# Kernel tuning notes

Measured on AMD Instinct MI355X. Metric: run time of the kernel, lower is better.

Reference implementation:

```python
import jax, jax.numpy as jnp
import numpy as np

L, B, IN, H, OUT = 4, 4096, 1024, 1024, 1024


def setup_inputs() -> dict:
    key = jax.random.key(0)
    ks = jax.random.split(key, 9)
    std = 1.0 / (H + IN) ** 0.5
    return {
        "x": jax.random.normal(ks[0], (B, IN), jnp.float32),
        "h_prev": jax.random.normal(ks[1], (L, B, H), jnp.float32),
        "c_prev": jax.random.normal(ks[2], (L, B, H), jnp.float32),
        "Wi": jax.random.uniform(ks[3], (L, IN, 4 * H), jnp.float32, -std, std),
        "Wh": jax.random.uniform(ks[4], (L, H, 4 * H), jnp.float32, -std, std),
        "bi": jax.random.uniform(ks[5], (L, 4 * H), jnp.float32, -std, std),
        "bh": jax.random.uniform(ks[6], (L, 4 * H), jnp.float32, -std, std),
        "fc_W": jax.random.uniform(ks[7], (H, OUT), jnp.float32, -std, std),
        "fc_b": jax.random.uniform(ks[8], (OUT,), jnp.float32, -std, std),
    }


def _lstm_cell(x, h, c, Wi, Wh, bi, bh):
    # gates: [B, 4H], split into (input, forget, cell, output)
    gates = x @ Wi + bi + h @ Wh + bh
    i, f, g, o = jnp.split(gates, 4, axis=1)
    i, f, o = jax.nn.sigmoid(i), jax.nn.sigmoid(f), jax.nn.sigmoid(o)
    g = jnp.tanh(g)
    c_cur = f * c + i * g
    h_cur = o * jnp.tanh(c_cur)
    return h_cur, c_cur


def reference(x, h_prev, c_prev, Wi, Wh, bi, bh, fc_W, fc_b):
    h_out, c_out = [], []
    x_in = x
    for l in range(L):  # fixed small layer loop
        h_cur, c_cur = _lstm_cell(x_in, h_prev[l], c_prev[l], Wi[l], Wh[l], bi[l], bh[l])
        h_out.append(h_cur)
        c_out.append(c_cur)
        x_in = h_cur
    h_out = jnp.stack(h_out, axis=0)
    c_out = jnp.stack(c_out, axis=0)
    y = h_out[-1] @ fc_W + fc_b
    return y, h_out, c_out
```

## Files before the change

### kernel.cpp

```cpp
#include <hip/hip_runtime.h>

#define B_    4096
#define H_    1024
#define NLAY  4

typedef __attribute__((ext_vector_type(8))) short bf16x8;
typedef __attribute__((ext_vector_type(4))) short s16x4;
typedef __attribute__((ext_vector_type(4))) float f32x4;
typedef unsigned short ushort_t;

__device__ __forceinline__ ushort_t f2bf(float f) {
  unsigned u = __builtin_bit_cast(unsigned, f);
  u += 0x7FFFu + ((u >> 16) & 1u);
  return (ushort_t)(u >> 16);
}

__device__ __forceinline__ float fast_sigmoid(float x) {
  float e = __expf(-fabsf(x));
  float s = 1.0f / (1.0f + e);
  return x >= 0.0f ? s : 1.0f - s;
}
__device__ __forceinline__ float fast_tanh(float x) {
  float e = __expf(-2.0f * fabsf(x));
  float t = (1.0f - e) / (1.0f + e);
  return x >= 0.0f ? t : -t;
}

#define GLDS16(gsrc, ldst)                                                  \
  __builtin_amdgcn_global_load_lds(                                         \
      (__attribute__((address_space(1))) void*)(gsrc),                      \
      (__attribute__((address_space(3))) void*)(ldst), 16, 0, 0)

#define BAR()                                                               \
  { asm volatile("" ::: "memory");                                          \
    __builtin_amdgcn_s_barrier();                                           \
    asm volatile("" ::: "memory"); }

#define WAITV(N)                                                            \
  { asm volatile("s_waitcnt vmcnt(" #N ")" ::: "memory");                   \
    __builtin_amdgcn_sched_barrier(0); }

#define LGKM0()                                                             \
  { asm volatile("s_waitcnt lgkmcnt(0)" ::: "memory");                      \
    __builtin_amdgcn_sched_barrier(0); }

__device__ __forceinline__ bf16x8 dsr128(unsigned addr, int imm) {
  bf16x8 r;
  asm volatile("ds_read_b128 %0, %1 offset:%c2"
               : "=v"(r)
               : "v"(addr), "i"(imm));
  return r;
}

__global__ __launch_bounds__(256, 1) void lstm8(
    const ushort_t* __restrict__ aX, const ushort_t* __restrict__ aH,
    const float* __restrict__ cprev, const float* __restrict__ bi,
    const float* __restrict__ bh, const ushort_t* __restrict__ wtl,
    float* __restrict__ hout, float* __restrict__ cout,
    ushort_t* __restrict__ hbfout) {
  __shared__ __align__(16) char sL[131072];

  const int tid  = threadIdx.x;
  const int lane = tid & 63;
  const int wid  = tid >> 6;
  const int wm   = wid >> 1;
  const int wn   = wid & 1;
  const int xcd = blockIdx.x & 7, bj = blockIdx.x >> 3;
  const int bm  = (xcd >> 2) * 8 + (bj >> 2);
  const int bn  = (xcd & 3) * 4 + (bj & 3);

  const int fr = lane & 15;
  const int oF = lane >> 4;
  const int sw = (oF ^ ((fr >> 1) & 3)) * 16;

  const unsigned sBase = (unsigned)(size_t)&sL[0];
  const unsigned aAddr = sBase + (unsigned)(wm * 16384 + fr * 64 + sw);
  const unsigned bAddr = sBase + (unsigned)(65536 + wn * 16384 + fr * 64 + sw);

  int aof[4];
#pragma unroll
  for (int c = 0; c < 4; ++c) {
    const int q = tid + c * 256;
    const int kh = q >> 9, r = (q >> 2) & 127, s = q & 3;
    const int o = s ^ ((r >> 1) & 3);
    aof[c] = r * 1024 + kh * 32 + o * 8;
  }
  const int aof0 = aof[0], aof1 = aof[1], aof2 = aof[2], aof3 = aof[3];
  const size_t aRowBase = (size_t)(bm * 256) * 1024;
  const ushort_t* wtBn = wtl + (size_t)bn * 524288;

  f32x4 acc[8][8];
#pragma unroll
  for (int m = 0; m < 8; ++m)
#pragma unroll
    for (int n = 0; n < 8; ++n) acc[m][n] = (f32x4){0.f, 0.f, 0.f, 0.f};

  bf16x8 ar[4][2], br0[4][2], br1[4][2];

#define STAGE_A(PAR, HALF, TT)                                               \
  {                                                                          \
    const ushort_t* bp = (((TT) < 16) ? aX : aH) + aRowBase +                \
                         (HALF) * 131072 + ((TT) & 15) * 64;                 \
    char* d = sL + (PAR) * 32768 + (HALF) * 16384 + wid * 1024;              \
    GLDS16(bp + aof0, d);                                                    \
    GLDS16(bp + aof1, d + 4096);                                             \
    GLDS16(bp + aof2, d + 8192);                                             \
    GLDS16(bp + aof3, d + 12288);                                            \
  }
#define STAGE_B(PAR, HALF, TT)                                               \
  {                                                                          \
    const ushort_t* bp =                                                     \
        wtBn + (size_t)(TT) * 16384 + (HALF) * 8192 + tid * 8;               \
    char* d = sL + 65536 + (PAR) * 32768 + (HALF) * 16384 + wid * 1024;      \
    GLDS16(bp, d);                                                           \
    GLDS16(bp + 2048, d + 4096);                                             \
    GLDS16(bp + 4096, d + 8192);                                             \
    GLDS16(bp + 6144, d + 12288);                                            \
  }
#define RD_A(PAR, MH)                                                        \
  _Pragma("unroll") for (int mp = 0; mp < 4; ++mp)                           \
      _Pragma("unroll") for (int kh = 0; kh < 2; ++kh)                       \
      ar[mp][kh] = dsr128(aAddr, (PAR) * 32768 + kh * 8192 +                 \
                                     ((MH) * 4 + mp) * 1024);
#define RD_B(PAR, NH, BR)                                                    \
  _Pragma("unroll") for (int gg = 0; gg < 4; ++gg)                           \
      _Pragma("unroll") for (int kh = 0; kh < 2; ++kh)                       \
      BR[gg][kh] = dsr128(bAddr, (PAR) * 32768 + kh * 8192 +                 \
                                     ((NH) * 4 + gg) * 1024);
#define MM(MH, NH, BR)                                                       \
  _Pragma("unroll") for (int gg = 0; gg < 4; ++gg)                           \
      _Pragma("unroll") for (int mp = 0; mp < 4; ++mp)                       \
      _Pragma("unroll") for (int kh = 0; kh < 2; ++kh)                       \
      acc[(MH) * 4 + mp][(NH) * 4 + gg] =                                    \
          __builtin_amdgcn_mfma_f32_16x16x32_bf16(                           \
              ar[mp][kh], BR[gg][kh], acc[(MH) * 4 + mp][(NH) * 4 + gg],     \
              0, 0, 0);

  STAGE_A(0, 0, 0)
  STAGE_A(0, 1, 0)
  STAGE_B(0, 0, 0)
  STAGE_B(0, 1, 0)
  STAGE_B(1, 0, 1)
  STAGE_B(1, 1, 1)
  WAITV(8)
  BAR()

#pragma unroll 1
  for (int t2 = 0; t2 < 32; t2 += 2) {
    RD_A(0, 0) RD_B(0, 0, br0)
    STAGE_A(1, 0, t2 + 1)
    BAR()
    LGKM0()
    MM(0, 0, br0)
    BAR()

    RD_B(0, 1, br1)
    STAGE_A(1, 1, t2 + 1)
    BAR()
    LGKM0()
    MM(0, 1, br1)
    BAR()

    RD_A(0, 1)
    STAGE_B(0, 0, t2 + 2)
    BAR()
    LGKM0()
    MM(1, 0, br0)
    BAR()

    STAGE_B(0, 1, t2 + 2)
    BAR()
    MM(1, 1, br1)
    WAITV(8)
    BAR()

    RD_A(1, 0) RD_B(1, 0, br0)
    STAGE_A(0, 0, t2 + 2)
    BAR()
    LGKM0()
    MM(0, 0, br0)
    BAR()

    RD_B(1, 1, br1)
    STAGE_A(0, 1, t2 + 2)
    BAR()
    LGKM0()
    MM(0, 1, br1)
    BAR()

    RD_A(1, 1)
    STAGE_B(1, 0, t2 + 3)
    BAR()
    LGKM0()
    MM(1, 0, br0)
    BAR()

    STAGE_B(1, 1, t2 + 3)
    BAR()
    MM(1, 1, br1)
    WAITV(8)
    BAR()
  }
#undef STAGE_A
#undef STAGE_B
#undef RD_A
#undef RD_B
#undef MM

  WAITV(0)
  __syncthreads();

  float bsum[2][4];
#pragma unroll
  for (int hg = 0; hg < 2; ++hg)
#pragma unroll
    for (int g = 0; g < 4; ++g) {
      const int col = g * 1024 + bn * 64 + wn * 32 + hg * 16 + fr;
      bsum[hg][g] = bi[col] + bh[col];
    }

#define LSTRIDE 68
  float* LF = (float*)sL;
  const int crow = tid >> 4;
  const int cc4  = (tid & 15) * 4;
  {
    const float* cp0 = cprev + (size_t)(bm * 256) * 1024 + bn * 64;
#pragma unroll
    for (int i = 0; i < 16; ++i) {
      const int row = i * 16 + crow;
      f32x4 v = *(const f32x4*)(cp0 + (size_t)row * 1024 + cc4);
      *(f32x4*)(LF + row * LSTRIDE + cc4) = v;
    }
  }
  __syncthreads();
  float hv[8][2][4];
#pragma unroll
  for (int m = 0; m < 8; ++m) {
    const int rowb = wm * 128 + m * 16 + oF * 4;
#pragma unroll
    for (int hg = 0; hg < 2; ++hg) {
      const int hc = wn * 32 + hg * 16 + fr;
#pragma unroll
      for (int r = 0; r < 4; ++r) {
        const float cp = LF[(rowb + r) * LSTRIDE + hc];
        const float gi = fast_sigmoid(acc[m][0 + hg][r] + bsum[hg][0]);
        const float gf = fast_sigmoid(acc[m][2 + hg][r] + bsum[hg][1]);
        const float gg = fast_tanh(acc[m][4 + hg][r] + bsum[hg][2]);
        const float go = fast_sigmoid(acc[m][6 + hg][r] + bsum[hg][3]);
        const float c  = gf * cp + gi * gg;
        LF[(rowb + r) * LSTRIDE + hc] = c;
        hv[m][hg][r] = go * fast_tanh(c);
      }
    }
  }
  __syncthreads();
  {
    float* co0 = cout + (size_t)(bm * 256) * 1024 + bn * 64;
#pragma unroll
    for (int i = 0; i < 16; ++i) {
      const int row = i * 16 + crow;
      f32x4 v = *(const f32x4*)(LF + row * LSTRIDE + cc4);
      *(f32x4*)(co0 + (size_t)row * 1024 + cc4) = v;
    }
  }
  __syncthreads();
#pragma unroll
  for (int m = 0; m < 8; ++m) {
    const int rowb = wm * 128 + m * 16 + oF * 4;
#pragma unroll
    for (int hg = 0; hg < 2; ++hg) {
      const int hc = wn * 32 + hg * 16 + fr;
#pragma unroll
      for (int r = 0; r < 4; ++r) LF[(rowb + r) * LSTRIDE + hc] = hv[m][hg][r];
    }
  }
  __syncthreads();
  {
    float* ho0 = hout + (size_t)(bm * 256) * 1024 + bn * 64;
    ushort_t* hb0 = hbfout + (size_t)(bm * 256) * 1024 + bn * 64;
#pragma unroll
    for (int i = 0; i < 16; ++i) {
      const int row = i * 16 + crow;
      f32x4 v = *(const f32x4*)(LF + row * LSTRIDE + cc4);
      *(f32x4*)(ho0 + (size_t)row * 1024 + cc4) = v;
      s16x4 hb;
#pragma unroll
      for (int j = 0; j < 4; ++j) hb[j] = (short)f2bf(v[j]);
      *(s16x4*)(hb0 + (size_t)row * 1024 + cc4) = hb;
    }
  }
#undef LSTRIDE
}

__global__ __launch_bounds__(512) void packW(const float* __restrict__ Wi,
                                             const float* __restrict__ Wh,
                                             ushort_t* __restrict__ wt) {
  __shared__ ushort_t t16[64 * 256];
  const int bn = blockIdx.x;
  const int T  = blockIdx.y;
  const int l  = blockIdx.z;
  const int tid = threadIdx.x;
  const int kq = tid >> 6, cc = tid & 63;
  const int k0 = T * 64;
  const float* W = (k0 < 1024)
                       ? (Wi + (size_t)l * 1024 * 4096 + (size_t)k0 * 4096)
                       : (Wh + (size_t)l * 1024 * 4096 + (size_t)(k0 - 1024) * 4096);
#pragma unroll
  for (int kk = 0; kk < 8; ++kk) {
    const int kl = kq * 8 + kk;
#pragma unroll
    for (int g = 0; g < 4; ++g) {
      const float v = W[(size_t)kl * 4096 + g * 1024 + bn * 64 + cc];
      const int p = (cc >> 5) * 128 + g * 32 + ((cc >> 4) & 1) * 16 + (cc & 15);
      t16[kl * 256 + p] = f2bf(v);
    }
  }
  __syncthreads();
  ushort_t* tile = wt + (((size_t)l * 16 + bn) * 32 + T) * 16384;
#pragma unroll
  for (int c = 0; c < 4; ++c) {
    const int idx = c * 512 + tid;
    const int half = idx >> 10;
    const int kh = (idx >> 9) & 1;
    const int r  = (idx >> 2) & 127;
    const int s  = idx & 3;
    const int o  = s ^ ((r >> 1) & 3);
    const int klb = kh * 32 + o * 8;
    const int p   = half * 128 + r;
    bf16x8 ov;
#pragma unroll
    for (int j = 0; j < 8; ++j) ov[j] = (short)t16[(klb + j) * 256 + p];
    *(bf16x8*)(tile + (size_t)idx * 8) = ov;
  }
}

__device__ __forceinline__ int swz(int row, int kelem) {
  return ((row * 64 + kelem) * 2) ^ ((row & 7) << 4);
}

__global__ __launch_bounds__(512) void fc_kernel(
    const ushort_t* __restrict__ wtfc, const ushort_t* __restrict__ abf,
    const float* __restrict__ bias, float* __restrict__ y) {
  __shared__ __align__(16) char sA[128 * 64 * 2];
  __shared__ __align__(16) char sB[64 * 64 * 2];
  const int tid  = threadIdx.x;
  const int lane = tid & 63;
  const int wid  = tid >> 6;
  const int wm   = wid >> 2;
  const int wn   = wid & 3;
  const int bid  = (blockIdx.x & 7) * 64 + (blockIdx.x >> 3);
  const int bm   = bid & 31;
  const int bn   = bid >> 5;

  f32x4 acc[4];
#pragma unroll
  for (int m = 0; m < 4; ++m) acc[m] = (f32x4){0.f, 0.f, 0.f, 0.f};

  const int rloc = wid * 8 + (lane >> 3);
  const int jA   = (lane & 7) ^ ((lane >> 3) & 7);
  const ushort_t* aSrc = abf + (size_t)(bm * 128 + rloc) * 1024 + jA * 8;

  for (int ks = 0; ks < 16; ++ks) {
    __syncthreads();
    GLDS16(wtfc + (size_t)(bn * 16 + ks) * 4096 + tid * 8, sB + wid * 1024);
    const int off = ks * 64;
    GLDS16(aSrc + off,             sA + wid * 1024);
    GLDS16(aSrc + off + 64 * 1024, sA + 8192 + wid * 1024);
    __syncthreads();
#pragma unroll
    for (int kk = 0; kk < 64; kk += 32) {
      const int ke = kk + (lane >> 4) * 8;
      bf16x8 a[4];
#pragma unroll
      for (int m = 0; m < 4; ++m)
        a[m] = *(const bf16x8*)(sA + swz(wm * 64 + m * 16 + (lane & 15), ke));
      bf16x8 b = *(const bf16x8*)(sB + swz(wn * 16 + (lane & 15), ke));
#pragma unroll
      for (int m = 0; m < 4; ++m)
        acc[m] = __builtin_amdgcn_mfma_f32_16x16x32_bf16(a[m], b, acc[m], 0, 0, 0);
    }
  }
  const int col = bn * 64 + wn * 16 + (lane & 15);
  const float bb = bias[col];
#pragma unroll
  for (int m = 0; m < 4; ++m) {
    const int row0 = bm * 128 + wm * 64 + m * 16 + ((lane >> 4) << 2);
#pragma unroll
    for (int r = 0; r < 4; ++r)
      y[(size_t)(row0 + r) * 1024 + col] = acc[m][r] + bb;
  }
}

__global__ __launch_bounds__(512) void transposeFc(const float* __restrict__ W,
                                                   ushort_t* __restrict__ wt) {
  const int bn = blockIdx.x;
  const int ks = blockIdx.y;
  const int tid = threadIdx.x;
  const int c  = tid & 63;
  const int ko = (tid >> 6) * 8;
  float v[8];
#pragma unroll
  for (int j = 0; j < 8; ++j)
    v[j] = W[(size_t)(ks * 64 + ko + j) * 1024 + bn * 64 + c];
  bf16x8 o;
#pragma unroll
  for (int j = 0; j < 8; ++j) o[j] = (short)f2bf(v[j]);
  ushort_t* tile = wt + ((size_t)bn * 16 + ks) * 4096;
  *(bf16x8*)((char*)tile + swz(c, ko)) = o;
}

__global__ __launch_bounds__(256) void cvt_bf16(const float* __restrict__ s,
                                                ushort_t* __restrict__ d,
                                                int n8) {
  const int i = blockIdx.x * 256 + threadIdx.x;
  if (i >= n8) return;
  const float* p = s + (size_t)i * 8;
  f32x4 a = ((const f32x4*)p)[0];
  f32x4 b = ((const f32x4*)p)[1];
  bf16x8 o;
#pragma unroll
  for (int j = 0; j < 4; ++j) {
    o[j]     = (short)f2bf(a[j]);
    o[4 + j] = (short)f2bf(b[j]);
  }
  *(bf16x8*)(d + (size_t)i * 8) = o;
}

extern "C" void kernel_launch(void* const* d_in, const int* in_sizes, int n_in,
                              void* d_out, int out_size, void* d_ws,
                              size_t ws_size, hipStream_t stream) {
  const float* x     = (const float*)d_in[0];
  const float* hprev = (const float*)d_in[1];
  const float* cprev = (const float*)d_in[2];
  const float* Wi    = (const float*)d_in[3];
  const float* Wh    = (const float*)d_in[4];
  const float* bi    = (const float*)d_in[5];
  const float* bh    = (const float*)d_in[6];
  const float* fcW   = (const float*)d_in[7];
  const float* fcb   = (const float*)d_in[8];

  float* out = (float*)d_out;
  const size_t BH = (size_t)B_ * H_;
  float* y    = out;
  float* hout = out + BH;
  float* cout = out + 5 * BH;

  const size_t WT_ELEMS = (size_t)4 * 16 * 32 * 16384;
  const size_t FC_ELEMS = (size_t)16 * 16 * 4096;
  ushort_t* wt      = (ushort_t*)d_ws;
  ushort_t* fcwt    = wt + WT_ELEMS;
  ushort_t* xbf     = fcwt + FC_ELEMS;
  ushort_t* hprevbf = xbf + BH;
  ushort_t* houtbf  = hprevbf + 4 * BH;

  packW<<<dim3(16, 32, 4), dim3(512), 0, stream>>>(Wi, Wh, wt);
  transposeFc<<<dim3(16, 16), dim3(512), 0, stream>>>(fcW, fcwt);
  cvt_bf16<<<dim3((int)(BH / 8 / 256)), dim3(256), 0, stream>>>(x, xbf,
                                                                (int)(BH / 8));
  cvt_bf16<<<dim3((int)(4 * BH / 8 / 256)), dim3(256), 0, stream>>>(
      hprev, hprevbf, (int)(4 * BH / 8));

  for (int l = 0; l < NLAY; ++l) {
    const ushort_t* aX  = (l == 0) ? xbf : (houtbf + (size_t)(l - 1) * BH);
    const ushort_t* wtl = wt + (size_t)l * 16 * 32 * 16384;
    lstm8<<<dim3(256), dim3(256), 0, stream>>>(
        aX, hprevbf + (size_t)l * BH, cprev + (size_t)l * BH, bi + l * 4096,
        bh + l * 4096, wtl, hout + (size_t)l * BH, cout + (size_t)l * BH,
        houtbf + (size_t)l * BH);
  }
  fc_kernel<<<dim3(512), dim3(512), 0, stream>>>(fcwt, houtbf + 3 * BH, fcb, y);
}
```

Baseline: 446.3 us.

## Merge prep kernels, pad packW LDS, triple-buffer fc, pin LSTM accumulators to AGPRs

The fc weight transpose is folded into packW as an extra z-slice, and the two bf16 conversion launches are merged into one kernel, cutting the launch count. packW's shared-memory tile row stride is padded from 256 to 257 to reduce bank conflicts. fc_kernel gains a three-stage global-to-LDS prefetch pipeline in place of its sync-load-sync loop. The lstm8 MFMAs are issued through inline asm with accumulators constrained to AGPRs, which may change register allocation and scheduling freedom.

```diff
diff --git a/kernel.cpp b/kernel.cpp
--- a/kernel.cpp
+++ b/kernel.cpp
@@ -50,6 +50,16 @@
                : "=v"(r)
                : "v"(addr), "i"(imm));
   return r;
+}
+
+__device__ __forceinline__ void mfma_a(f32x4& d, bf16x8 a, bf16x8 b) {
+  asm volatile("v_mfma_f32_16x16x32_bf16 %0, %1, %2, %0"
+               : "+a"(d)
+               : "v"(a), "v"(b));
+}
+
+__device__ __forceinline__ int swz(int row, int kelem) {
+  return ((row * 64 + kelem) * 2) ^ ((row & 7) << 4);
 }
 
 __global__ __launch_bounds__(256, 1) void lstm8(
@@ -131,10 +141,7 @@
   _Pragma("unroll") for (int gg = 0; gg < 4; ++gg)                           \
       _Pragma("unroll") for (int mp = 0; mp < 4; ++mp)                       \
       _Pragma("unroll") for (int kh = 0; kh < 2; ++kh)                       \
-      acc[(MH) * 4 + mp][(NH) * 4 + gg] =                                    \
-          __builtin_amdgcn_mfma_f32_16x16x32_bf16(                           \
-              ar[mp][kh], BR[gg][kh], acc[(MH) * 4 + mp][(NH) * 4 + gg],     \
-              0, 0, 0);
+      mfma_a(acc[(MH) * 4 + mp][(NH) * 4 + gg], ar[mp][kh], BR[gg][kh]);
 
   STAGE_A(0, 0, 0)
   STAGE_A(0, 1, 0)
@@ -294,12 +301,31 @@
 
 __global__ __launch_bounds__(512) void packW(const float* __restrict__ Wi,
                                              const float* __restrict__ Wh,
-                                             ushort_t* __restrict__ wt) {
-  __shared__ ushort_t t16[64 * 256];
+                                             const float* __restrict__ Wfc,
+                                             ushort_t* __restrict__ wt,
+                                             ushort_t* __restrict__ fcwt) {
   const int bn = blockIdx.x;
   const int T  = blockIdx.y;
   const int l  = blockIdx.z;
   const int tid = threadIdx.x;
+
+  if (l == 4) {
+    if (T >= 16) return;
+    const int c  = tid & 63;
+    const int ko = (tid >> 6) * 8;
+    float v[8];
+#pragma unroll
+    for (int j = 0; j < 8; ++j)
+      v[j] = Wfc[(size_t)(T * 64 + ko + j) * 1024 + bn * 64 + c];
+    bf16x8 o;
+#pragma unroll
+    for (int j = 0; j < 8; ++j) o[j] = (short)f2bf(v[j]);
+    ushort_t* tile = fcwt + ((size_t)bn * 16 + T) * 4096;
+    *(bf16x8*)((char*)tile + swz(c, ko)) = o;
+    return;
+  }
+
+  __shared__ ushort_t t16[64 * 257];
   const int kq = tid >> 6, cc = tid & 63;
   const int k0 = T * 64;
   const float* W = (k0 < 1024)
@@ -312,7 +338,7 @@
     for (int g = 0; g < 4; ++g) {
       const float v = W[(size_t)kl * 4096 + g * 1024 + bn * 64 + cc];
       const int p = (cc >> 5) * 128 + g * 32 + ((cc >> 4) & 1) * 16 + (cc & 15);
-      t16[kl * 256 + p] = f2bf(v);
+      t16[kl * 257 + p] = f2bf(v);
     }
   }
   __syncthreads();
@@ -329,20 +355,16 @@
     const int p   = half * 128 + r;
     bf16x8 ov;
 #pragma unroll
-    for (int j = 0; j < 8; ++j) ov[j] = (short)t16[(klb + j) * 256 + p];
+    for (int j = 0; j < 8; ++j) ov[j] = (short)t16[(klb + j) * 257 + p];
     *(bf16x8*)(tile + (size_t)idx * 8) = ov;
   }
-}
-
-__device__ __forceinline__ int swz(int row, int kelem) {
-  return ((row * 64 + kelem) * 2) ^ ((row & 7) << 4);
 }
 
 __global__ __launch_bounds__(512) void fc_kernel(
     const ushort_t* __restrict__ wtfc, const ushort_t* __restrict__ abf,
     const float* __restrict__ bias, float* __restrict__ y) {
-  __shared__ __align__(16) char sA[128 * 64 * 2];
-  __shared__ __align__(16) char sB[64 * 64 * 2];
+  __shared__ __align__(16) char sA[3][16384];
+  __shared__ __align__(16) char sB[3][8192];
   const int tid  = threadIdx.x;
   const int lane = tid & 63;
   const int wid  = tid >> 6;
@@ -360,26 +382,43 @@
   const int jA   = (lane & 7) ^ ((lane >> 3) & 7);
   const ushort_t* aSrc = abf + (size_t)(bm * 128 + rloc) * 1024 + jA * 8;
 
+#define FSTAGE(BUF, KS)                                                      \
+  {                                                                          \
+    GLDS16(wtfc + (size_t)(bn * 16 + (KS)) * 4096 + tid * 8,                 \
+           sB[BUF] + wid * 1024);                                            \
+    GLDS16(aSrc + (KS) * 64, sA[BUF] + wid * 1024);                          \
+    GLDS16(aSrc + (KS) * 64 + 64 * 1024, sA[BUF] + 8192 + wid * 1024);       \
+  }
+
+  FSTAGE(0, 0)
+  FSTAGE(1, 1)
+  WAITV(3)
+  BAR()
+
+#pragma unroll
   for (int ks = 0; ks < 16; ++ks) {
-    __syncthreads();
-    GLDS16(wtfc + (size_t)(bn * 16 + ks) * 4096 + tid * 8, sB + wid * 1024);
-    const int off = ks * 64;
-    GLDS16(aSrc + off,             sA + wid * 1024);
-    GLDS16(aSrc + off + 64 * 1024, sA + 8192 + wid * 1024);
-    __syncthreads();
+    const int cur = ks % 3;
+    if (ks + 2 < 16) { FSTAGE((ks + 2) % 3, ks + 2) }
 #pragma unroll
     for (int kk = 0; kk < 64; kk += 32) {
       const int ke = kk + (lane >> 4) * 8;
       bf16x8 a[4];
 #pragma unroll
       for (int m = 0; m < 4; ++m)
-        a[m] = *(const bf16x8*)(sA + swz(wm * 64 + m * 16 + (lane & 15), ke));
-      bf16x8 b = *(const bf16x8*)(sB + swz(wn * 16 + (lane & 15), ke));
+        a[m] = *(const bf16x8*)(sA[cur] +
+                                swz(wm * 64 + m * 16 + (lane & 15), ke));
+      bf16x8 b = *(const bf16x8*)(sB[cur] + swz(wn * 16 + (lane & 15), ke));
 #pragma unroll
       for (int m = 0; m < 4; ++m)
         acc[m] = __builtin_amdgcn_mfma_f32_16x16x32_bf16(a[m], b, acc[m], 0, 0, 0);
     }
-  }
+    if (ks < 15) {
+      if (ks + 2 < 16) { WAITV(3) } else { WAITV(0) }
+      BAR()
+    }
+  }
+#undef FSTAGE
+
   const int col = bn * 64 + wn * 16 + (lane & 15);
   const float bb = bias[col];
 #pragma unroll
@@ -391,39 +430,32 @@
   }
 }
 
-__global__ __launch_bounds__(512) void transposeFc(const float* __restrict__ W,
-                                                   ushort_t* __restrict__ wt) {
-  const int bn = blockIdx.x;
-  const int ks = blockIdx.y;
-  const int tid = threadIdx.x;
-  const int c  = tid & 63;
-  const int ko = (tid >> 6) * 8;
-  float v[8];
-#pragma unroll
-  for (int j = 0; j < 8; ++j)
-    v[j] = W[(size_t)(ks * 64 + ko + j) * 1024 + bn * 64 + c];
+__global__ __launch_bounds__(256) void cvt_bf16_2(const float* __restrict__ s0,
+                                                  unsigned n0,
+                                                  const float* __restrict__ s1,
+                                                  ushort_t* __restrict__ d0,
+                                                  ushort_t* __restrict__ d1,
+                                                  unsigned ntot) {
+  const unsigned i = blockIdx.x * 256 + threadIdx.x;
+  if (i >= ntot) return;
+  const float* p;
+  ushort_t* d;
+  unsigned j;
+  if (i < n0) {
+    p = s0; d = d0; j = i;
+  } else {
+    p = s1; d = d1; j = i - n0;
+  }
+  const float* pp = p + (size_t)j * 8;
+  f32x4 a = ((const f32x4*)pp)[0];
+  f32x4 b = ((const f32x4*)pp)[1];
   bf16x8 o;
 #pragma unroll
-  for (int j = 0; j < 8; ++j) o[j] = (short)f2bf(v[j]);
-  ushort_t* tile = wt + ((size_t)bn * 16 + ks) * 4096;
-  *(bf16x8*)((char*)tile + swz(c, ko)) = o;
-}
-
-__global__ __launch_bounds__(256) void cvt_bf16(const float* __restrict__ s,
-                                                ushort_t* __restrict__ d,
-                                                int n8) {
-  const int i = blockIdx.x * 256 + threadIdx.x;
-  if (i >= n8) return;
-  const float* p = s + (size_t)i * 8;
-  f32x4 a = ((const f32x4*)p)[0];
-  f32x4 b = ((const f32x4*)p)[1];
-  bf16x8 o;
-#pragma unroll
-  for (int j = 0; j < 4; ++j) {
-    o[j]     = (short)f2bf(a[j]);
-    o[4 + j] = (short)f2bf(b[j]);
-  }
-  *(bf16x8*)(d + (size_t)i * 8) = o;
+  for (int k = 0; k < 4; ++k) {
+    o[k]     = (short)f2bf(a[k]);
+    o[4 + k] = (short)f2bf(b[k]);
+  }
+  *(bf16x8*)(d + (size_t)j * 8) = o;
 }
 
 extern "C" void kernel_launch(void* const* d_in, const int* in_sizes, int n_in,
@@ -453,12 +485,14 @@
   ushort_t* hprevbf = xbf + BH;
   ushort_t* houtbf  = hprevbf + 4 * BH;
 
-  packW<<<dim3(16, 32, 4), dim3(512), 0, stream>>>(Wi, Wh, wt);
-  transposeFc<<<dim3(16, 16), dim3(512), 0, stream>>>(fcW, fcwt);
-  cvt_bf16<<<dim3((int)(BH / 8 / 256)), dim3(256), 0, stream>>>(x, xbf,
-                                                                (int)(BH / 8));
-  cvt_bf16<<<dim3((int)(4 * BH / 8 / 256)), dim3(256), 0, stream>>>(
-      hprev, hprevbf, (int)(4 * BH / 8));
+  packW<<<dim3(16, 32, 5), dim3(512), 0, stream>>>(Wi, Wh, fcW, wt, fcwt);
+  {
+    const unsigned n0 = (unsigned)(BH / 8);
+    const unsigned n1 = (unsigned)(4 * BH / 8);
+    const unsigned nt = n0 + n1;
+    cvt_bf16_2<<<dim3((nt + 255) / 256), dim3(256), 0, stream>>>(
+        x, n0, hprev, xbf, hprevbf, nt);
+  }
 
   for (int l = 0; l < NLAY; ++l) {
     const ushort_t* aX  = (l == 0) ? xbf : (houtbf + (size_t)(l - 1) * BH);
```

Measured after the change: 399.2 us. 1.12x faster.
